# Kernel tuning notes

Measured on AMD Instinct MI355X. Metric: run time of the kernel, lower is better.

Reference implementation:

```python
import jax, jax.numpy as jnp
import numpy as np
from jax.scipy.linalg import solve_triangular

B, T, D, H, DK = 32, 256, 2048, 16, 64  # batch, chunk len, hidden, heads, head_dim


def setup_inputs() -> dict:
    key = jax.random.key(0)
    ks = jax.random.split(key, 7)
    s = 1.0 / np.sqrt(D)
    g = jnp.linspace(0.8, 0.999, H)
    return {
        'W_old': jax.random.normal(ks[0], (B, H, DK, DK), jnp.float32) * 0.02,
        'content': jax.random.normal(ks[1], (B, T, D), jnp.float32),
        'k_w': jax.random.normal(ks[2], (H * DK, D), jnp.float32) * s,
        'v_w': jax.random.normal(ks[3], (H * DK, D), jnp.float32) * s,
        'b_w': jax.random.normal(ks[4], (H, D), jnp.float32) * s,
        'b_b': jnp.zeros((H,), jnp.float32),
        'ts_w': jax.random.normal(ks[5], (H, D), jnp.float32) * 0.02,
        'ts_b': jnp.zeros((H,), jnp.float32),
        'hd_logits': jnp.log(g / (1.0 - g)).astype(jnp.float32),
    }


def _delta_write(W_old, content, k_w, v_w, b_w, b_b, ts_w, ts_b, hd_logits):
    # projections: (B,T,D) -> (B,H,T,d)
    k = (content @ k_w.T).reshape(B, T, H, DK).transpose(0, 2, 1, 3)
    v = (content @ v_w.T).reshape(B, T, H, DK).transpose(0, 2, 1, 3)
    k = k / jnp.clip(jnp.linalg.norm(k, axis=-1, keepdims=True), 1e-12)  # L2 normalize
    beta = jax.nn.sigmoid(content @ b_w.T + b_b).transpose(0, 2, 1)        # (B,H,T)
    gamma = jax.nn.sigmoid(hd_logits + content @ ts_w.T + ts_b).transpose(0, 2, 1)  # (B,H,T)

    # log-space prefix products of gamma
    log_gamma = jnp.log(jnp.clip(gamma, 1e-8))
    cum_log = jnp.cumsum(log_gamma, axis=-1)                               # (B,H,T)
    cum_log_im1 = jnp.pad(cum_log[..., :-1], ((0, 0), (0, 0), (1, 0)))     # G_{i-1}, G_0=1
    log_ratio = jnp.minimum(cum_log_im1[..., :, None] - cum_log[..., None, :], 0.0)
    ratio = jnp.exp(log_ratio)                                             # (B,H,T,T)
    G_im1 = jnp.exp(cum_log_im1)
    G_T = jnp.exp(cum_log[..., -1:])                                       # (B,H,1)

    # RHS: v_i - G_{i-1} W0 k_i
    W0k = jnp.einsum('bhvd,bhtd->bhtv', W_old, k)
    V_rhs = v - G_im1[..., None] * W0k

    # strictly-lower triangular system (I + A) V' = V_rhs
    KK = jnp.einsum('bhid,bhjd->bhij', k, k)
    A = beta[..., None, :] * ratio * KK
    tril = jnp.tril(jnp.ones((T, T), bool), k=-1)
    L = jnp.eye(T, dtype=A.dtype) + jnp.where(tril, A, 0.0)
    Vp = solve_triangular(L, V_rhs, lower=True, unit_diagonal=True)        # (B,H,T,d_v)

    decay_to_T = jnp.exp(cum_log[..., -1:] - cum_log)                      # (B,H,T)
    weighted = (beta * decay_to_T)[..., None] * Vp
    W_new = G_T[..., None] * W_old + jnp.einsum('bhtv,bhtd->bhvd', weighted, k)
    return W_new


def reference(W_old, content, k_w, v_w, b_w, b_b, ts_w, ts_b, hd_logits):
    return _delta_write(W_old, content, k_w, v_w, b_w, b_b, ts_w, ts_b, hd_logits)
```

## Files before the change

kernel.cpp:

```cpp
#include <hip/hip_runtime.h>
#include <hip/hip_bf16.h>
#include <math.h>

constexpr int B = 32, T = 256, D = 2048, H = 16, DK = 64;
constexpr size_t BHTD = (size_t)B * H * T * DK;
constexpr int NC8 = (B * T * D) / 8;
constexpr int NW8 = (H * DK * D) / 8;
constexpr int NB8 = (H * D) / 8;

typedef __attribute__((ext_vector_type(8))) short short8;
typedef __attribute__((ext_vector_type(4))) float f32x4;

#define MFMA16(a, b, c) __builtin_amdgcn_mfma_f32_16x16x32_bf16((a), (b), (c), 0, 0, 0)

__global__ __launch_bounds__(256) void cast_all(
    const float* __restrict__ content, const float* __restrict__ k_w,
    const float* __restrict__ v_w, const float* __restrict__ b_w,
    const float* __restrict__ ts_w, __hip_bfloat16* __restrict__ c_bf,
    __hip_bfloat16* __restrict__ w_bf) {
  const int total = NC8 + 2 * NW8 + 2 * NB8;
  int i = blockIdx.x * blockDim.x + threadIdx.x;
  const int stride = gridDim.x * blockDim.x;
  for (; i < total; i += stride) {
    const float* src;
    __hip_bfloat16* dst;
    int idx;
    if (i < NC8) { src = content; dst = c_bf; idx = i; }
    else if (i < NC8 + NW8) { src = k_w; dst = w_bf; idx = i - NC8; }
    else if (i < NC8 + 2 * NW8) {
      src = v_w; dst = w_bf + (size_t)1024 * D; idx = i - NC8 - NW8;
    } else if (i < NC8 + 2 * NW8 + NB8) {
      src = b_w; dst = w_bf + (size_t)2048 * D; idx = i - NC8 - 2 * NW8;
    } else {
      src = ts_w; dst = w_bf + (size_t)2064 * D; idx = i - NC8 - 2 * NW8 - NB8;
    }
    const float4 x = ((const float4*)src)[2 * idx];
    const float4 y = ((const float4*)src)[2 * idx + 1];
    __hip_bfloat16 tmp[8];
    tmp[0] = __float2bfloat16(x.x); tmp[1] = __float2bfloat16(x.y);
    tmp[2] = __float2bfloat16(x.z); tmp[3] = __float2bfloat16(x.w);
    tmp[4] = __float2bfloat16(y.x); tmp[5] = __float2bfloat16(y.y);
    tmp[6] = __float2bfloat16(y.z); tmp[7] = __float2bfloat16(y.w);
    *(uint4*)(dst + 8 * (size_t)idx) = *(const uint4*)tmp;
  }
}

__device__ __forceinline__ short8 ldsfrag128(const char* half_base, int row, int g) {
  return *(const short8*)(half_base + row * 128 + ((g ^ (row & 7)) << 4));
}

#define GBAR()                                   \
  do {                                           \
    asm volatile("" ::: "memory");               \
    __builtin_amdgcn_sched_barrier(0);           \
    __builtin_amdgcn_s_barrier();                \
    __builtin_amdgcn_sched_barrier(0);           \
  } while (0)

__global__ __launch_bounds__(512, 2) void gemm256(
    const __hip_bfloat16* __restrict__ A, const __hip_bfloat16* __restrict__ Wc,
    float* __restrict__ outk) {
  extern __shared__ char smem[];
  const int tid = threadIdx.x;
  const int w = tid >> 6, l = tid & 63;
  const int wm = w >> 2, wn = w & 3;
  const int fr = l & 15, fq = l >> 4;
  const int x = blockIdx.x & 7, q = (blockIdx.x >> 3) & 3, nt = blockIdx.x >> 5;
  const int mt = x * 4 + q;
  const int m0 = mt * 256, n0 = nt * 256;
  const int lrow = l >> 3;
  const int lg = ((l & 7) ^ lrow) * 8;

  auto stage = [&](const __hip_bfloat16* gbase, char* lds_half) {
#pragma unroll
    for (int r = 0; r < 2; ++r) {
      __builtin_amdgcn_global_load_lds(
          (const __attribute__((address_space(1))) void*)(
              gbase + (size_t)(r * 64 + w * 8 + lrow) * D + lg),
          (__attribute__((address_space(3))) void*)(lds_half + r * 8192 + w * 1024),
          16, 0, 0);
    }
  };
  auto issue = [&](int h) {
    if (h >= 128) return;
    const int tau = h >> 2, s = h & 3;
    const int k0 = tau * 64;
    char* base = smem + ((s < 2) ? 65536 : 0) + ((tau & 1) * 2 + (s & 1)) * 16384;
    const __hip_bfloat16* g = (s < 2)
        ? (Wc + (size_t)(n0 + (s & 1) * 128) * D + k0)
        : (A + (size_t)(m0 + (s & 1) * 128) * D + k0);
    stage(g, base);
  };

  for (int h = 0; h < 7; ++h) issue(h);
  asm volatile("s_waitcnt vmcnt(6)" ::: "memory");
  GBAR();

  f32x4 acc[8][4] = {};
  for (int tau = 0; tau < 32; ++tau) {
    const char* Ah = smem + ((tau & 1) * 2 + wm) * 16384;
    const char* Bh = smem + 65536 + ((tau & 1) * 2 + (wn >> 1)) * 16384;
    const int br0 = (wn & 1) * 64;
    short8 b0[4], b1[4], aA[2], aB[2], aC[2], aD[2];

#pragma unroll
    for (int j = 0; j < 4; ++j) {
      b0[j] = ldsfrag128(Bh, br0 + j * 16 + fr, fq);
      b1[j] = ldsfrag128(Bh, br0 + j * 16 + fr, 4 + fq);
    }
#pragma unroll
    for (int kk = 0; kk < 2; ++kk) {
      aA[kk] = ldsfrag128(Ah, 0 * 16 + fr, kk * 4 + fq);
      aB[kk] = ldsfrag128(Ah, 1 * 16 + fr, kk * 4 + fq);
    }
    issue(4 * tau + 7);
    GBAR();
    asm volatile("s_waitcnt lgkmcnt(0)" ::: "memory");
    __builtin_amdgcn_sched_barrier(0);
    __builtin_amdgcn_s_setprio(1);
#pragma unroll
    for (int j = 0; j < 4; ++j) {
      acc[0][j] = MFMA16(aA[0], b0[j], acc[0][j]);
      acc[0][j] = MFMA16(aA[1], b1[j], acc[0][j]);
      acc[1][j] = MFMA16(aB[0], b0[j], acc[1][j]);
      acc[1][j] = MFMA16(aB[1], b1[j], acc[1][j]);
    }
    __builtin_amdgcn_s_setprio(0);
    GBAR();

#pragma unroll
    for (int kk = 0; kk < 2; ++kk) {
      aA[kk] = ldsfrag128(Ah, 2 * 16 + fr, kk * 4 + fq);
      aB[kk] = ldsfrag128(Ah, 3 * 16 + fr, kk * 4 + fq);
    }
    issue(4 * tau + 8);
    GBAR();
    asm volatile("s_waitcnt lgkmcnt(0)" ::: "memory");
    __builtin_amdgcn_sched_barrier(0);
    __builtin_amdgcn_s_setprio(1);
#pragma unroll
    for (int j = 0; j < 4; ++j) {
      acc[2][j] = MFMA16(aA[0], b0[j], acc[2][j]);
      acc[2][j] = MFMA16(aA[1], b1[j], acc[2][j]);
      acc[3][j] = MFMA16(aB[0], b0[j], acc[3][j]);
      acc[3][j] = MFMA16(aB[1], b1[j], acc[3][j]);
    }
    __builtin_amdgcn_s_setprio(0);
    GBAR();

#pragma unroll
    for (int kk = 0; kk < 2; ++kk) {
      aA[kk] = ldsfrag128(Ah, 4 * 16 + fr, kk * 4 + fq);
      aB[kk] = ldsfrag128(Ah, 5 * 16 + fr, kk * 4 + fq);
      aC[kk] = ldsfrag128(Ah, 6 * 16 + fr, kk * 4 + fq);
      aD[kk] = ldsfrag128(Ah, 7 * 16 + fr, kk * 4 + fq);
    }
    issue(4 * tau + 9);
    GBAR();
    asm volatile("s_waitcnt lgkmcnt(0)" ::: "memory");
    __builtin_amdgcn_sched_barrier(0);
    __builtin_amdgcn_s_setprio(1);
#pragma unroll
    for (int j = 0; j < 4; ++j) {
      acc[4][j] = MFMA16(aA[0], b0[j], acc[4][j]);
      acc[4][j] = MFMA16(aA[1], b1[j], acc[4][j]);
      acc[5][j] = MFMA16(aB[0], b0[j], acc[5][j]);
      acc[5][j] = MFMA16(aB[1], b1[j], acc[5][j]);
    }
    __builtin_amdgcn_s_setprio(0);
    GBAR();

    issue(4 * tau + 10);
    GBAR();
    __builtin_amdgcn_s_setprio(1);
#pragma unroll
    for (int j = 0; j < 4; ++j) {
      acc[6][j] = MFMA16(aC[0], b0[j], acc[6][j]);
      acc[6][j] = MFMA16(aC[1], b1[j], acc[6][j]);
      acc[7][j] = MFMA16(aD[0], b0[j], acc[7][j]);
      acc[7][j] = MFMA16(aD[1], b1[j], acc[7][j]);
    }
    __builtin_amdgcn_s_setprio(0);
    if (tau < 30) asm volatile("s_waitcnt vmcnt(6)" ::: "memory");
    else asm volatile("s_waitcnt vmcnt(0)" ::: "memory");
    GBAR();
  }

#pragma unroll
  for (int i = 0; i < 8; ++i) {
    const int mbase = m0 + wm * 128 + i * 16 + fq * 4;
#pragma unroll
    for (int j = 0; j < 4; ++j) {
      const int n = n0 + wn * 64 + j * 16 + fr;
      const int h = (n >> 6) & 15, dk = n & 63;
      float* dst = outk + (size_t)(n >> 10) * BHTD;
#pragma unroll
      for (int r = 0; r < 4; ++r) {
        const int mm = mbase + r;
        const int b = mm >> 8, t = mm & 255;
        dst[(((size_t)b * H + h) * T + t) * DK + dk] = acc[i][j][r];
      }
    }
  }
}

__global__ __launch_bounds__(128) void bg_gemm(
    const __hip_bfloat16* __restrict__ A, const __hip_bfloat16* __restrict__ Wbg,
    const float* __restrict__ b_b, const float* __restrict__ ts_b,
    const float* __restrict__ hd, float* __restrict__ beta_out,
    float* __restrict__ gamma_out) {
  const int tid = threadIdx.x, w = tid >> 6, l = tid & 63;
  const int fr = l & 15, fq = l >> 4;
  const int m0 = blockIdx.x * 32 + w * 16;
  f32x4 acc0 = {0.f, 0.f, 0.f, 0.f}, acc1 = {0.f, 0.f, 0.f, 0.f};
  const __hip_bfloat16* ar = A + (size_t)(m0 + fr) * D + fq * 8;
  const __hip_bfloat16* br = Wbg + (size_t)fr * D + fq * 8;
  const __hip_bfloat16* gr = Wbg + (size_t)(16 + fr) * D + fq * 8;
#pragma unroll 4
  for (int k0 = 0; k0 < D; k0 += 32) {
    short8 af = *(const short8*)(ar + k0);
    short8 bfb = *(const short8*)(br + k0);
    short8 bfg = *(const short8*)(gr + k0);
    acc0 = MFMA16(af, bfb, acc0);
    acc1 = MFMA16(af, bfg, acc1);
  }
  const float bb = b_b[fr], bg = ts_b[fr] + hd[fr];
#pragma unroll
  for (int r = 0; r < 4; ++r) {
    const int mm = m0 + fq * 4 + r;
    const int b = mm >> 8, t = mm & 255;
    const size_t oo = ((size_t)b * H + fr) * T + t;
    beta_out[oo] = 1.f / (1.f + __expf(-(acc0[r] + bb)));
    gamma_out[oo] = 1.f / (1.f + __expf(-(acc1[r] + bg)));
  }
}

__device__ __forceinline__ float rdlane(float x, int j) {
  return __int_as_float(__builtin_amdgcn_readlane(__float_as_int(x), j));
}
__device__ __forceinline__ int bofs(int row, int col) {
  return row * 128 + ((((col >> 3) ^ (row & 7))) << 4) + ((col & 7) << 1);
}
__device__ __forceinline__ short8 ldsfrag(const __hip_bfloat16* base, int row, int g0) {
  return *(const short8*)((const char*)base + row * 128 + (((g0 ^ (row & 7))) << 4));
}

__global__ __launch_bounds__(256, 2) void solve_write(
    const float* __restrict__ kg, const float* __restrict__ vg,
    const float* __restrict__ betag, const float* __restrict__ gammag,
    const float* __restrict__ Wold, float* __restrict__ Wnew) {
  __shared__ __hip_bfloat16 kCb[64 * 64];
  __shared__ __hip_bfloat16 kTb[64 * 64];
  __shared__ __hip_bfloat16 Mb[64 * 64];
  __shared__ __hip_bfloat16 Ub[64 * 64];
  __shared__ float Ss[64][68];
  __shared__ float Uu[64][68];
  __shared__ float s_beta[256], s_cl[256];
  __shared__ float wpart[4];

  const int tid = threadIdx.x;
  const int bh = blockIdx.x;
  const size_t base = (size_t)bh * T * DK;
  const int lane = tid & 63, w = tid >> 6;
  const int fr = lane & 15, fq = lane >> 4;

  s_beta[tid] = betag[(size_t)bh * T + tid];
  float xls = __logf(fmaxf(gammag[(size_t)bh * T + tid], 1e-8f));
#pragma unroll
  for (int d = 1; d < 64; d <<= 1) {
    float y = __shfl_up(xls, d, 64);
    if (lane >= d) xls += y;
  }
  if (lane == 63) wpart[w] = xls;
  __syncthreads();
  {
    float off = 0.f;
    if (w > 0) off += wpart[0];
    if (w > 1) off += wpart[1];
    if (w > 2) off += wpart[2];
    s_cl[tid] = xls + off;
  }
  f32x4 mreg[4];
  {
    const float* Wo = Wold + (size_t)bh * DK * DK;
#pragma unroll
    for (int j = 0; j < 4; ++j)
#pragma unroll
      for (int r = 0; r < 4; ++r)
        mreg[j][r] = Wo[(size_t)(16 * w + fq * 4 + r) * DK + 16 * j + fr];
  }
  __syncthreads();

  for (int c = 0; c < 4; ++c) {
    const int c0 = c * 64;
    const float oc = (c == 0) ? 0.f : s_cl[c0 - 1];
    const float on = s_cl[c0 + 63];

    {
      const int r = tid >> 2, p = tid & 3;
      const float4* kp = (const float4*)(kg + base + (size_t)(c0 + r) * DK + p * 16);
      float4 x0 = kp[0], x1 = kp[1], x2 = kp[2], x3 = kp[3];
      float nrm = x0.x * x0.x + x0.y * x0.y + x0.z * x0.z + x0.w * x0.w +
                  x1.x * x1.x + x1.y * x1.y + x1.z * x1.z + x1.w * x1.w +
                  x2.x * x2.x + x2.y * x2.y + x2.z * x2.z + x2.w * x2.w +
                  x3.x * x3.x + x3.y * x3.y + x3.z * x3.z + x3.w * x3.w;
      nrm += __shfl_xor(nrm, 1, 64);
      nrm += __shfl_xor(nrm, 2, 64);
      const float rn = 1.f / fmaxf(sqrtf(nrm), 1e-12f);
      float kvf[16] = {x0.x * rn, x0.y * rn, x0.z * rn, x0.w * rn,
                       x1.x * rn, x1.y * rn, x1.z * rn, x1.w * rn,
                       x2.x * rn, x2.y * rn, x2.z * rn, x2.w * rn,
                       x3.x * rn, x3.y * rn, x3.z * rn, x3.w * rn};
      short kb[16];
#pragma unroll
      for (int u = 0; u < 16; ++u) {
        __hip_bfloat16 h = __float2bfloat16(kvf[u]);
        kb[u] = *(short*)&h;
      }
      *(short8*)((char*)kCb + r * 128 + (((2 * p) ^ (r & 7)) << 4)) = *(short8*)&kb[0];
      *(short8*)((char*)kCb + r * 128 + (((2 * p + 1) ^ (r & 7)) << 4)) = *(short8*)&kb[8];
#pragma unroll
      for (int u = 0; u < 16; ++u)
        *(short*)((char*)kTb + bofs(16 * p + u, r)) = kb[u];
#pragma unroll
      for (int j = 0; j < 4; ++j)
#pragma unroll
        for (int rr = 0; rr < 4; ++rr) {
          __hip_bfloat16 h = __float2bfloat16(mreg[j][rr]);
          *(short*)((char*)Mb + bofs(16 * w + fq * 4 + rr, 16 * j + fr)) = *(short*)&h;
        }
    }
    __syncthreads();

    {
      const short8 af0 = ldsfrag(kCb, 16 * w + fr, fq);
      const short8 af1 = ldsfrag(kCb, 16 * w + fr, 4 + fq);
      const f32x4 zero = {0.f, 0.f, 0.f, 0.f};
#pragma unroll
      for (int j = 0; j < 4; ++j) {
        short8 b0 = ldsfrag(kCb, 16 * j + fr, fq);
        short8 b1 = ldsfrag(kCb, 16 * j + fr, 4 + fq);
        f32x4 s4 = MFMA16(af0, b0, zero);
        s4 = MFMA16(af1, b1, s4);
#pragma unroll
        for (int r = 0; r < 4; ++r) Ss[16 * w + fq * 4 + r][16 * j + fr] = s4[r];
      }
      float eci[4];
#pragma unroll
      for (int r = 0; r < 4; ++r) {
        const int gi = c0 + 16 * w + fq * 4 + r;
        eci[r] = __expf((gi == 0) ? 0.f : s_cl[gi - 1] - oc);
      }
#pragma unroll
      for (int j = 0; j < 4; ++j) {
        short8 m0 = ldsfrag(Mb, 16 * j + fr, fq);
        short8 m1 = ldsfrag(Mb, 16 * j + fr, 4 + fq);
        f32x4 u4 = MFMA16(af0, m0, zero);
        u4 = MFMA16(af1, m1, u4);
#pragma unroll
        for (int r = 0; r < 4; ++r) {
          const int t = 16 * w + fq * 4 + r;
          const float vv = vg[base + (size_t)(c0 + t) * DK + 16 * j + fr];
          Uu[t][16 * j + fr] = vv - eci[r] * u4[r];
        }
      }
    }
    __syncthreads();

    {
      const int gi = c0 + lane;
      const int v0 = w * 16;
      float rhs[16];
#pragma unroll
      for (int u = 0; u < 4; ++u)
        *(float4*)&rhs[4 * u] = *(const float4*)&Uu[lane][v0 + 4 * u];
      const float ci = (gi == 0) ? 0.f : s_cl[gi - 1] - oc;
      const float ecl = __expf(ci);
      const float wgt = s_beta[gi] * __expf(-(s_cl[gi] - oc));
      for (int j = 0; j < 63; ++j) {
        const float wj = rdlane(wgt, j);
        const float sv = Ss[j][lane];
        const float co = (lane > j) ? ecl * wj * sv : 0.f;
#pragma unroll
        for (int u = 0; u < 16; ++u) rhs[u] -= co * rdlane(rhs[u], j);
      }
      const float ul = wgt * __expf(on - oc);
#pragma unroll
      for (int u = 0; u < 16; ++u) {
        __hip_bfloat16 h = __float2bfloat16(ul * rhs[u]);
        *(short*)((char*)Ub + bofs(v0 + u, lane)) = *(short*)&h;
      }
    }
    __syncthreads();

    {
      const float rc = __expf(on - oc);
      const short8 a0 = ldsfrag(Ub, 16 * w + fr, fq);
      const short8 a1 = ldsfrag(Ub, 16 * w + fr, 4 + fq);
#pragma unroll
      for (int j = 0; j < 4; ++j) {
        short8 b0 = ldsfrag(kTb, 16 * j + fr, fq);
        short8 b1 = ldsfrag(kTb, 16 * j + fr, 4 + fq);
        f32x4 c4;
#pragma unroll
        for (int r = 0; r < 4; ++r) c4[r] = rc * mreg[j][r];
        c4 = MFMA16(a0, b0, c4);
        c4 = MFMA16(a1, b1, c4);
        mreg[j] = c4;
      }
    }
    __syncthreads();
  }
  {
    float* op = Wnew + (size_t)bh * DK * DK;
#pragma unroll
    for (int j = 0; j < 4; ++j)
#pragma unroll
      for (int r = 0; r < 4; ++r)
        op[(size_t)(16 * w + fq * 4 + r) * DK + 16 * j + fr] = mreg[j][r];
  }
}

extern "C" void kernel_launch(void* const* d_in, const int* in_sizes, int n_in,
                              void* d_out, int out_size, void* d_ws, size_t ws_size,
                              hipStream_t stream) {
  const float* W_old = (const float*)d_in[0];
  const float* content = (const float*)d_in[1];
  const float* k_w = (const float*)d_in[2];
  const float* v_w = (const float*)d_in[3];
  const float* b_w = (const float*)d_in[4];
  const float* b_b = (const float*)d_in[5];
  const float* ts_w = (const float*)d_in[6];
  const float* ts_b = (const float*)d_in[7];
  const float* hd = (const float*)d_in[8];
  float* out = (float*)d_out;

  float* ws_k = (float*)d_ws;
  float* ws_v = ws_k + BHTD;
  float* ws_beta = ws_v + BHTD;
  float* ws_gamma = ws_beta + (size_t)B * H * T;
  __hip_bfloat16* c_bf = (__hip_bfloat16*)(ws_gamma + (size_t)B * H * T);
  __hip_bfloat16* w_bf = c_bf + (size_t)B * T * D;

  static int attr_done = 0;
  if (!attr_done) {
    hipFuncSetAttribute(reinterpret_cast<const void*>(gemm256),
                        hipFuncAttributeMaxDynamicSharedMemorySize, 131072);
    attr_done = 1;
  }

  cast_all<<<2048, 256, 0, stream>>>(content, k_w, v_w, b_w, ts_w, c_bf, w_bf);
  gemm256<<<dim3(256), dim3(512), 131072, stream>>>(c_bf, w_bf, ws_k);
  bg_gemm<<<dim3(256), dim3(128), 0, stream>>>(c_bf, w_bf + (size_t)2048 * D,
                                               b_b, ts_b, hd, ws_beta, ws_gamma);
  solve_write<<<dim3(B * H), 256, 0, stream>>>(ws_k, ws_v, ws_beta, ws_gamma,
                                               W_old, out);
}
```

Before: 274.0 us.

## Fuse beta/gamma GEMM into cast kernel and prefetch k/v in solve

The separate bg_gemm launch is removed. Its work now runs in extra blocks of the cast kernel, which read the fp32 content and weights directly and convert them inline, so the bf16 copies of b_w/ts_w are no longer needed. In solve_write, the next chunk's k and v rows are prefetched into registers while the current chunk computes, and the W-to-Mb conversion moves ahead of the k normalization. __syncthreads is replaced by a custom barrier that waits only on LDS counters. The risks are higher register pressure and the cast blocks reading fp32 content a second time.

```diff
diff --git a/kernel.cpp b/kernel.cpp
--- a/kernel.cpp
+++ b/kernel.cpp
@@ -6,42 +6,75 @@
 constexpr size_t BHTD = (size_t)B * H * T * DK;
 constexpr int NC8 = (B * T * D) / 8;
 constexpr int NW8 = (H * DK * D) / 8;
-constexpr int NB8 = (H * D) / 8;
+constexpr int CAST_TOTAL = NC8 + 2 * NW8;
 
 typedef __attribute__((ext_vector_type(8))) short short8;
 typedef __attribute__((ext_vector_type(4))) float f32x4;
 
 #define MFMA16(a, b, c) __builtin_amdgcn_mfma_f32_16x16x32_bf16((a), (b), (c), 0, 0, 0)
 
-__global__ __launch_bounds__(256) void cast_all(
+__device__ __forceinline__ short8 cvt8(const float* p) {
+  const float4 x = ((const float4*)p)[0];
+  const float4 y = ((const float4*)p)[1];
+  __hip_bfloat16 t[8];
+  t[0] = __float2bfloat16(x.x); t[1] = __float2bfloat16(x.y);
+  t[2] = __float2bfloat16(x.z); t[3] = __float2bfloat16(x.w);
+  t[4] = __float2bfloat16(y.x); t[5] = __float2bfloat16(y.y);
+  t[6] = __float2bfloat16(y.z); t[7] = __float2bfloat16(y.w);
+  return *(const short8*)t;
+}
+
+__global__ __launch_bounds__(256) void cast_bg(
     const float* __restrict__ content, const float* __restrict__ k_w,
     const float* __restrict__ v_w, const float* __restrict__ b_w,
-    const float* __restrict__ ts_w, __hip_bfloat16* __restrict__ c_bf,
-    __hip_bfloat16* __restrict__ w_bf) {
-  const int total = NC8 + 2 * NW8 + 2 * NB8;
-  int i = blockIdx.x * blockDim.x + threadIdx.x;
-  const int stride = gridDim.x * blockDim.x;
-  for (; i < total; i += stride) {
-    const float* src;
-    __hip_bfloat16* dst;
-    int idx;
-    if (i < NC8) { src = content; dst = c_bf; idx = i; }
-    else if (i < NC8 + NW8) { src = k_w; dst = w_bf; idx = i - NC8; }
-    else if (i < NC8 + 2 * NW8) {
-      src = v_w; dst = w_bf + (size_t)1024 * D; idx = i - NC8 - NW8;
-    } else if (i < NC8 + 2 * NW8 + NB8) {
-      src = b_w; dst = w_bf + (size_t)2048 * D; idx = i - NC8 - 2 * NW8;
-    } else {
-      src = ts_w; dst = w_bf + (size_t)2064 * D; idx = i - NC8 - 2 * NW8 - NB8;
-    }
-    const float4 x = ((const float4*)src)[2 * idx];
-    const float4 y = ((const float4*)src)[2 * idx + 1];
-    __hip_bfloat16 tmp[8];
-    tmp[0] = __float2bfloat16(x.x); tmp[1] = __float2bfloat16(x.y);
-    tmp[2] = __float2bfloat16(x.z); tmp[3] = __float2bfloat16(x.w);
-    tmp[4] = __float2bfloat16(y.x); tmp[5] = __float2bfloat16(y.y);
-    tmp[6] = __float2bfloat16(y.z); tmp[7] = __float2bfloat16(y.w);
-    *(uint4*)(dst + 8 * (size_t)idx) = *(const uint4*)tmp;
+    const float* __restrict__ ts_w, const float* __restrict__ b_b,
+    const float* __restrict__ ts_b, const float* __restrict__ hd,
+    __hip_bfloat16* __restrict__ c_bf, __hip_bfloat16* __restrict__ w_bf,
+    float* __restrict__ beta_out, float* __restrict__ gamma_out) {
+  const int bid = blockIdx.x;
+  if (bid < 2048) {
+    int i = bid * 256 + threadIdx.x;
+    for (; i < CAST_TOTAL; i += 2048 * 256) {
+      const float* src;
+      __hip_bfloat16* dst;
+      int idx;
+      if (i < NC8) { src = content; dst = c_bf; idx = i; }
+      else if (i < NC8 + NW8) { src = k_w; dst = w_bf; idx = i - NC8; }
+      else { src = v_w; dst = w_bf + (size_t)1024 * D; idx = i - NC8 - NW8; }
+      const float4 x = ((const float4*)src)[2 * idx];
+      const float4 y = ((const float4*)src)[2 * idx + 1];
+      __hip_bfloat16 tmp[8];
+      tmp[0] = __float2bfloat16(x.x); tmp[1] = __float2bfloat16(x.y);
+      tmp[2] = __float2bfloat16(x.z); tmp[3] = __float2bfloat16(x.w);
+      tmp[4] = __float2bfloat16(y.x); tmp[5] = __float2bfloat16(y.y);
+      tmp[6] = __float2bfloat16(y.z); tmp[7] = __float2bfloat16(y.w);
+      *(uint4*)(dst + 8 * (size_t)idx) = *(const uint4*)tmp;
+    }
+    return;
+  }
+  const int tid = threadIdx.x, w = tid >> 6, l = tid & 63;
+  const int fr = l & 15, fq = l >> 4;
+  const int m0 = (bid - 2048) * 64 + w * 16;
+  f32x4 acc0 = {0.f, 0.f, 0.f, 0.f}, acc1 = {0.f, 0.f, 0.f, 0.f};
+  const float* ar = content + (size_t)(m0 + fr) * D + fq * 8;
+  const float* br = b_w + (size_t)fr * D + fq * 8;
+  const float* gr = ts_w + (size_t)fr * D + fq * 8;
+#pragma unroll 4
+  for (int k0 = 0; k0 < D; k0 += 32) {
+    short8 af = cvt8(ar + k0);
+    short8 bfb = cvt8(br + k0);
+    short8 bfg = cvt8(gr + k0);
+    acc0 = MFMA16(af, bfb, acc0);
+    acc1 = MFMA16(af, bfg, acc1);
+  }
+  const float bb = b_b[fr], bg = ts_b[fr] + hd[fr];
+#pragma unroll
+  for (int r = 0; r < 4; ++r) {
+    const int mm = m0 + fq * 4 + r;
+    const int b = mm >> 8, t = mm & 255;
+    const size_t oo = ((size_t)b * H + fr) * T + t;
+    beta_out[oo] = 1.f / (1.f + __expf(-(acc0[r] + bb)));
+    gamma_out[oo] = 1.f / (1.f + __expf(-(acc1[r] + bg)));
   }
 }
 
@@ -204,37 +237,6 @@
   }
 }
 
-__global__ __launch_bounds__(128) void bg_gemm(
-    const __hip_bfloat16* __restrict__ A, const __hip_bfloat16* __restrict__ Wbg,
-    const float* __restrict__ b_b, const float* __restrict__ ts_b,
-    const float* __restrict__ hd, float* __restrict__ beta_out,
-    float* __restrict__ gamma_out) {
-  const int tid = threadIdx.x, w = tid >> 6, l = tid & 63;
-  const int fr = l & 15, fq = l >> 4;
-  const int m0 = blockIdx.x * 32 + w * 16;
-  f32x4 acc0 = {0.f, 0.f, 0.f, 0.f}, acc1 = {0.f, 0.f, 0.f, 0.f};
-  const __hip_bfloat16* ar = A + (size_t)(m0 + fr) * D + fq * 8;
-  const __hip_bfloat16* br = Wbg + (size_t)fr * D + fq * 8;
-  const __hip_bfloat16* gr = Wbg + (size_t)(16 + fr) * D + fq * 8;
-#pragma unroll 4
-  for (int k0 = 0; k0 < D; k0 += 32) {
-    short8 af = *(const short8*)(ar + k0);
-    short8 bfb = *(const short8*)(br + k0);
-    short8 bfg = *(const short8*)(gr + k0);
-    acc0 = MFMA16(af, bfb, acc0);
-    acc1 = MFMA16(af, bfg, acc1);
-  }
-  const float bb = b_b[fr], bg = ts_b[fr] + hd[fr];
-#pragma unroll
-  for (int r = 0; r < 4; ++r) {
-    const int mm = m0 + fq * 4 + r;
-    const int b = mm >> 8, t = mm & 255;
-    const size_t oo = ((size_t)b * H + fr) * T + t;
-    beta_out[oo] = 1.f / (1.f + __expf(-(acc0[r] + bb)));
-    gamma_out[oo] = 1.f / (1.f + __expf(-(acc1[r] + bg)));
-  }
-}
-
 __device__ __forceinline__ float rdlane(float x, int j) {
   return __int_as_float(__builtin_amdgcn_readlane(__float_as_int(x), j));
 }
@@ -244,6 +246,14 @@
 __device__ __forceinline__ short8 ldsfrag(const __hip_bfloat16* base, int row, int g0) {
   return *(const short8*)((const char*)base + row * 128 + (((g0 ^ (row & 7))) << 4));
 }
+
+#define SBAR()                                           \
+  do {                                                   \
+    __builtin_amdgcn_sched_barrier(0);                   \
+    asm volatile("s_waitcnt lgkmcnt(0)" ::: "memory");   \
+    __builtin_amdgcn_s_barrier();                        \
+    __builtin_amdgcn_sched_barrier(0);                   \
+  } while (0)
 
 __global__ __launch_bounds__(256, 2) void solve_write(
     const float* __restrict__ kg, const float* __restrict__ vg,
@@ -263,6 +273,7 @@
   const size_t base = (size_t)bh * T * DK;
   const int lane = tid & 63, w = tid >> 6;
   const int fr = lane & 15, fq = lane >> 4;
+  const int sr = tid >> 2, sp = tid & 3;
 
   s_beta[tid] = betag[(size_t)bh * T + tid];
   float xls = __logf(fmaxf(gammag[(size_t)bh * T + tid], 1e-8f));
@@ -289,7 +300,16 @@
       for (int r = 0; r < 4; ++r)
         mreg[j][r] = Wo[(size_t)(16 * w + fq * 4 + r) * DK + 16 * j + fr];
   }
-  __syncthreads();
+  const float4* kgp = (const float4*)(kg + base + (size_t)sr * DK) + sp * 4;
+  const float* vbase = vg + base + (size_t)(16 * w + fq * 4) * DK + fr;
+  float4 kx0 = kgp[0], kx1 = kgp[1], kx2 = kgp[2], kx3 = kgp[3];
+  float vv[16];
+#pragma unroll
+  for (int j = 0; j < 4; ++j)
+#pragma unroll
+    for (int r = 0; r < 4; ++r)
+      vv[4 * j + r] = vbase[(size_t)r * DK + 16 * j];
+  SBAR();
 
   for (int c = 0; c < 4; ++c) {
     const int c0 = c * 64;
@@ -297,9 +317,14 @@
     const float on = s_cl[c0 + 63];
 
     {
-      const int r = tid >> 2, p = tid & 3;
-      const float4* kp = (const float4*)(kg + base + (size_t)(c0 + r) * DK + p * 16);
-      float4 x0 = kp[0], x1 = kp[1], x2 = kp[2], x3 = kp[3];
+#pragma unroll
+      for (int j = 0; j < 4; ++j)
+#pragma unroll
+        for (int rr = 0; rr < 4; ++rr) {
+          __hip_bfloat16 h = __float2bfloat16(mreg[j][rr]);
+          *(short*)((char*)Mb + bofs(16 * w + fq * 4 + rr, 16 * j + fr)) = *(short*)&h;
+        }
+      const float4 x0 = kx0, x1 = kx1, x2 = kx2, x3 = kx3;
       float nrm = x0.x * x0.x + x0.y * x0.y + x0.z * x0.z + x0.w * x0.w +
                   x1.x * x1.x + x1.y * x1.y + x1.z * x1.z + x1.w * x1.w +
                   x2.x * x2.x + x2.y * x2.y + x2.z * x2.z + x2.w * x2.w +
@@ -317,20 +342,13 @@
         __hip_bfloat16 h = __float2bfloat16(kvf[u]);
         kb[u] = *(short*)&h;
       }
-      *(short8*)((char*)kCb + r * 128 + (((2 * p) ^ (r & 7)) << 4)) = *(short8*)&kb[0];
-      *(short8*)((char*)kCb + r * 128 + (((2 * p + 1) ^ (r & 7)) << 4)) = *(short8*)&kb[8];
+      *(short8*)((char*)kCb + sr * 128 + (((2 * sp) ^ (sr & 7)) << 4)) = *(short8*)&kb[0];
+      *(short8*)((char*)kCb + sr * 128 + (((2 * sp + 1) ^ (sr & 7)) << 4)) = *(short8*)&kb[8];
 #pragma unroll
       for (int u = 0; u < 16; ++u)
-        *(short*)((char*)kTb + bofs(16 * p + u, r)) = kb[u];
-#pragma unroll
-      for (int j = 0; j < 4; ++j)
-#pragma unroll
-        for (int rr = 0; rr < 4; ++rr) {
-          __hip_bfloat16 h = __float2bfloat16(mreg[j][rr]);
-          *(short*)((char*)Mb + bofs(16 * w + fq * 4 + rr, 16 * j + fr)) = *(short*)&h;
-        }
-    }
-    __syncthreads();
+        *(short*)((char*)kTb + bofs(16 * sp + u, sr)) = kb[u];
+    }
+    SBAR();
 
     {
       const short8 af0 = ldsfrag(kCb, 16 * w + fr, fq);
@@ -360,12 +378,21 @@
 #pragma unroll
         for (int r = 0; r < 4; ++r) {
           const int t = 16 * w + fq * 4 + r;
-          const float vv = vg[base + (size_t)(c0 + t) * DK + 16 * j + fr];
-          Uu[t][16 * j + fr] = vv - eci[r] * u4[r];
+          Uu[t][16 * j + fr] = vv[4 * j + r] - eci[r] * u4[r];
         }
       }
-    }
-    __syncthreads();
+      if (c < 3) {
+        const float4* kn = kgp + (size_t)(c + 1) * 1024;
+        kx0 = kn[0]; kx1 = kn[1]; kx2 = kn[2]; kx3 = kn[3];
+        const float* vn = vbase + (size_t)(c0 + 64) * DK;
+#pragma unroll
+        for (int j = 0; j < 4; ++j)
+#pragma unroll
+          for (int r = 0; r < 4; ++r)
+            vv[4 * j + r] = vn[(size_t)r * DK + 16 * j];
+      }
+    }
+    SBAR();
 
     {
       const int gi = c0 + lane;
@@ -391,7 +418,7 @@
         *(short*)((char*)Ub + bofs(v0 + u, lane)) = *(short*)&h;
       }
     }
-    __syncthreads();
+    SBAR();
 
     {
       const float rc = __expf(on - oc);
@@ -409,7 +436,7 @@
         mreg[j] = c4;
       }
     }
-    __syncthreads();
+    SBAR();
   }
   {
     float* op = Wnew + (size_t)bh * DK * DK;
@@ -449,10 +476,10 @@
     attr_done = 1;
   }
 
-  cast_all<<<2048, 256, 0, stream>>>(content, k_w, v_w, b_w, ts_w, c_bf, w_bf);
+  cast_bg<<<dim3(2176), 256, 0, stream>>>(content, k_w, v_w, b_w, ts_w,
+                                          b_b, ts_b, hd, c_bf, w_bf,
+                                          ws_beta, ws_gamma);
   gemm256<<<dim3(256), dim3(512), 131072, stream>>>(c_bf, w_bf, ws_k);
-  bg_gemm<<<dim3(256), dim3(128), 0, stream>>>(c_bf, w_bf + (size_t)2048 * D,
-                                               b_b, ts_b, hd, ws_beta, ws_gamma);
   solve_write<<<dim3(B * H), 256, 0, stream>>>(ws_k, ws_v, ws_beta, ws_gamma,
                                                W_old, out);
 }
```

Result: slower. 342.6 us (+25.1%).
